# Optimization experiments

Measured on AMD Instinct MI355X. Metric: run time of the kernel, lower is better.

## Reference

```python
import jax, jax.numpy as jnp
from jax import lax
import numpy as np

B = 2048; IMG = 28; K = 3; CIN = 1; HC = 32; LC = 16; WID = 64; HID = 64
LIS = IMG - 3 * (K - 1)           # 22: latent image size
FLAT = LIS * LIS * HC             # 15488
BLK = WID * LC                    # 1024: hypernet block size
T1 = 10.0; T0 = 0.0; NSTEP = 20   # fixed-step RK4 replaces adaptive dopri5
VAR = 0.1                         # p_z0 diagonal covariance


def _conv(x, w, b):  # w: [Cout,Cin,k,k], VALID conv, stride 1
    y = lax.conv_general_dilated(x, w, (1, 1), 'VALID',
                                 dimension_numbers=('NCHW', 'OIHW', 'NCHW'))
    return y + b[None, :, None, None]


def _convT(x, w, b):  # w: [Cin,Cout,k,k] (pytorch ConvTranspose2d layout)
    wf = jnp.flip(w, (2, 3)).transpose(1, 0, 2, 3)  # -> OIHW, spatially flipped
    y = lax.conv_general_dilated(x, wf, (1, 1), [(K - 1, K - 1), (K - 1, K - 1)],
                                 dimension_numbers=('NCHW', 'OIHW', 'NCHW'))
    return y + b[None, :, None, None]


def _forward(x, c0w, c0b, c1w, c1b, c2w, c2b, elw, elb, dlw, dlb,
             t0w, t0b, t1w, t1b, t2w, t2b, h1w, h1b, h2w, h2b, h3w, h3b):
    # ---- encoder (dropout in eval = identity) ----
    h = jnp.tanh(_conv(x, c0w, c0b))
    h = jnp.tanh(_conv(h, c1w, c1b))
    h = jnp.tanh(_conv(h, c2w, c2b))
    z1 = h.reshape(h.shape[0], -1) @ elw + elb          # [B, LC]
    # ---- decoder ----
    d = jnp.tanh(z1 @ dlw + dlb)                         # [B, FLAT]
    d = d.reshape(-1, HC, LIS, LIS)
    d = jnp.tanh(_convT(d, t0w, t0b))
    d = jnp.tanh(_convT(d, t1w, t1b))
    recon = _convT(d, t2w, t2b)                          # [B, CIN, 28, 28]

    # ---- CNF vector field with analytic trace ----
    def hyper(t):
        p = jnp.tanh(jnp.reshape(jnp.asarray(t, jnp.float32), (1, 1)) @ h1w + h1b)
        p = jnp.tanh(p @ h2w + h2b)
        p = (p @ h3w + h3b).reshape(-1)
        W = p[:BLK].reshape(WID, LC)
        U = p[BLK:2 * BLK].reshape(WID, LC) * jax.nn.sigmoid(p[2 * BLK:3 * BLK].reshape(WID, LC))
        Bb = p[3 * BLK:]                                 # [WID]
        return W, Bb, U

    def f(t, z):
        W, Bb, U = hyper(t)
        hh = jnp.tanh(jnp.einsum('bd,wd->wb', z, W) + Bb[:, None])   # [WID, B]
        dz = jnp.einsum('wb,wd->bd', hh, U) / WID                     # [B, LC]
        s = jnp.sum(W * U, axis=1)                                    # [WID]: sum_i W_w[i]U_w[i]
        tr = jnp.mean((1.0 - hh * hh) * s[:, None], axis=0)           # [B] analytic trace
        return dz, -tr[:, None]

    dt = (T0 - T1) / NSTEP

    def step(state, i):
        z, lp = state
        t = T1 + i * dt
        k1z, k1l = f(t, z)
        k2z, k2l = f(t + 0.5 * dt, z + 0.5 * dt * k1z)
        k3z, k3l = f(t + 0.5 * dt, z + 0.5 * dt * k2z)
        k4z, k4l = f(t + dt, z + dt * k3z)
        z = z + dt / 6.0 * (k1z + 2 * k2z + 2 * k3z + k4z)
        lp = lp + dt / 6.0 * (k1l + 2 * k2l + 2 * k3l + k4l)
        return (z, lp), None

    lp1 = jnp.zeros((z1.shape[0], 1), z1.dtype)
    (z0, lp0), _ = lax.scan(step, (z1, lp1), jnp.arange(NSTEP, dtype=jnp.float32))

    # MultivariateNormal(0, 0.1*I) log_prob
    logp = -0.5 * (LC * jnp.log(2 * jnp.pi) + LC * jnp.log(VAR) + jnp.sum(z0 * z0, -1) / VAR)
    x_probs = jnp.mean(logp - lp0[:, 0])
    return recon, x_probs


def setup_inputs() -> dict:
    key = jax.random.key(0)
    ks = jax.random.split(key, 16)
    n = jax.random.normal
    s = jnp.float32(0.05)
    z = jnp.zeros
    OUT3 = 3 * BLK + WID
    return {
        'x': n(ks[0], (B, CIN, IMG, IMG), jnp.float32),
        'c0w': n(ks[1], (HC, CIN, K, K)) * s, 'c0b': z((HC,)),
        'c1w': n(ks[2], (HC, HC, K, K)) * s, 'c1b': z((HC,)),
        'c2w': n(ks[3], (HC, HC, K, K)) * s, 'c2b': z((HC,)),
        'elw': n(ks[4], (FLAT, LC)) * s, 'elb': z((LC,)),
        'dlw': n(ks[5], (LC, FLAT)) * s, 'dlb': z((FLAT,)),
        't0w': n(ks[6], (HC, HC, K, K)) * s, 't0b': z((HC,)),
        't1w': n(ks[7], (HC, HC, K, K)) * s, 't1b': z((HC,)),
        't2w': n(ks[8], (HC, CIN, K, K)) * s, 't2b': z((CIN,)),
        'h1w': n(ks[9], (1, HID)) * s, 'h1b': z((HID,)),
        'h2w': n(ks[10], (HID, HID)) * s, 'h2b': z((HID,)),
        'h3w': n(ks[11], (HID, OUT3)) * s, 'h3b': z((OUT3,)),
    }


def reference(x, c0w, c0b, c1w, c1b, c2w, c2b, elw, elb, dlw, dlb,
              t0w, t0b, t1w, t1b, t2w, t2b, h1w, h1b, h2w, h2b, h3w, h3b):
    return _forward(x, c0w, c0b, c1w, c1b, c2w, c2b, elw, elb, dlw, dlb,
                    t0w, t0b, t1w, t1b, t2w, t2b, h1w, h1b, h2w, h2b, h3w, h3b)
```

## Files before the change

kernel.cpp:

```cpp
#include <hip/hip_runtime.h>
#include <math.h>

#define Bsz 2048

using bf16x8 = __attribute__((ext_vector_type(8))) short;
using f32x4  = __attribute__((ext_vector_type(4))) float;

__device__ __forceinline__ float fast_tanh(float x){
    float e = __expf(2.0f * x);
    return 1.0f - 2.0f / (e + 1.0f);
}
__device__ __forceinline__ float fast_sigmoid(float x){
    return 1.0f / (1.0f + __expf(-x));
}
__device__ __forceinline__ unsigned short f2b(float f){
    union { float f; unsigned u; } v; v.f = f;
    unsigned r = v.u + 0x7FFFu + ((v.u >> 16) & 1u);
    return (unsigned short)(r >> 16);
}
__device__ __forceinline__ float b2f(unsigned short s){
    union { unsigned u; float f; } v; v.u = ((unsigned)s) << 16;
    return v.f;
}

__device__ __forceinline__ float stage_t(int sidx){
    int i  = sidx >> 2, st = sidx & 3;
    float t = 10.0f - 0.5f * (float)i;
    if (st == 1 || st == 2) t -= 0.25f;
    else if (st == 3)       t -= 0.5f;
    return t;
}

__global__ void k_prep(const float* __restrict__ c1w, const float* __restrict__ c2w,
                       const float* __restrict__ t0w, const float* __restrict__ t1w,
                       const float* __restrict__ elw, const float* __restrict__ dlw,
                       const float* __restrict__ elb,
                       unsigned short* __restrict__ wc1, unsigned short* __restrict__ wc2,
                       unsigned short* __restrict__ wt0, unsigned short* __restrict__ wt1,
                       unsigned short* __restrict__ elwT, unsigned short* __restrict__ dlwT,
                       float* __restrict__ z1, int full){
    int gsz = gridDim.x * 256;
    for (int i = blockIdx.x*256 + threadIdx.x; i < 9216; i += gsz){
        int ci = i & 31, co = (i >> 5) & 31, s = i >> 10;
        wc1[i] = f2b(c1w[(co*32 + ci)*9 + s]);
        wc2[i] = f2b(c2w[(co*32 + ci)*9 + s]);
        wt0[i] = f2b(t0w[(ci*32 + co)*9 + (8 - s)]);
        wt1[i] = f2b(t1w[(ci*32 + co)*9 + (8 - s)]);
    }
    if (!full) return;
    for (int i = blockIdx.x*256 + threadIdx.x; i < 32768; i += gsz)
        z1[i] = elb[i & 15];
    for (int i = blockIdx.x*256 + threadIdx.x; i < 247808; i += gsz){
        int l = i / 15488, f2 = i - l*15488;
        int pos = f2 >> 5, ci = f2 & 31;
        elwT[i] = f2b(elw[(ci*484 + pos)*16 + l]);
    }
    for (int i = blockIdx.x*256 + threadIdx.x; i < 247808; i += gsz){
        int f2 = i >> 4, l = i & 15;
        int pos = f2 >> 5, ci = f2 & 31;
        dlwT[i] = f2b(dlw[l*15488 + ci*484 + pos]);
    }
}

__global__ void __launch_bounds__(256)
k_conv0(const float* __restrict__ x, const float* __restrict__ c0w,
        const float* __restrict__ c0b, unsigned short* __restrict__ A0,
        int cb, int CH){
    int gid = blockIdx.x*256 + threadIdx.x;
    if (gid >= CH*676) return;
    int b = gid / 676, pos = gid - b*676;
    int y = pos / 26, xx = pos - y*26;
    const float* xin = x + (size_t)(cb + b)*784;
    float v[9];
#pragma unroll
    for (int r = 0; r < 3; r++)
#pragma unroll
        for (int s = 0; s < 3; s++)
            v[r*3+s] = xin[(y+r)*28 + xx + s];
    unsigned short* ob = A0 + (size_t)b*21632 + pos*32;
#pragma unroll
    for (int g = 0; g < 8; g++){
        float a0 = c0b[g*4+0], a1 = c0b[g*4+1], a2 = c0b[g*4+2], a3 = c0b[g*4+3];
#pragma unroll
        for (int k = 0; k < 9; k++){
            a0 += v[k] * c0w[(g*4+0)*9 + k];
            a1 += v[k] * c0w[(g*4+1)*9 + k];
            a2 += v[k] * c0w[(g*4+2)*9 + k];
            a3 += v[k] * c0w[(g*4+3)*9 + k];
        }
        ushort4 o;
        o.x = f2b(fast_tanh(a0)); o.y = f2b(fast_tanh(a1));
        o.z = f2b(fast_tanh(a2)); o.w = f2b(fast_tanh(a3));
        *(ushort4*)(ob + g*4) = o;
    }
}

template<int IL, int OL, int OW, int OOFF, int INS, int OUTS>
__global__ void __launch_bounds__(256)
k_convM(const unsigned short* __restrict__ in, const unsigned short* __restrict__ wg,
        const float* __restrict__ bias, unsigned short* __restrict__ out, int CH){
    constexpr int N  = OL * OL;
    constexpr int NT = (N + 15) / 16;
    const int tid = threadIdx.x;
    const int wave = tid >> 6, lane = tid & 63;
    const int q = lane >> 4, nn = lane & 15;
    const int nw = gridDim.x * 4;

    bf16x8 af[2][9];
#pragma unroll
    for (int mt = 0; mt < 2; mt++)
#pragma unroll
        for (int s = 0; s < 9; s++)
            af[mt][s] = *(const bf16x8*)(wg + s*1024 + (mt*16 + nn)*32 + q*8);
    float4 bc0 = *(const float4*)(bias + q*4);
    float4 bc1 = *(const float4*)(bias + 16 + q*4);

    for (int t = blockIdx.x*4 + wave; t < CH*NT; t += nw){
        int img = t / NT, tt = t - img*NT;
        const unsigned short* inb = in + (size_t)img * INS;
        unsigned short* outb = out + (size_t)img * OUTS;
        int pos = tt*16 + nn;
        int pc  = pos < N ? pos : N - 1;
        int oy = pc / OL, ox = pc - oy*OL;
        const unsigned short* ib = inb + (oy*IL + ox)*32 + q*8;
        f32x4 acc0 = {0.f,0.f,0.f,0.f}, acc1 = {0.f,0.f,0.f,0.f};
#pragma unroll
        for (int r = 0; r < 3; r++){
            bf16x8 b0 = *(const bf16x8*)(ib + (r*IL + 0)*32);
            bf16x8 b1 = *(const bf16x8*)(ib + (r*IL + 1)*32);
            bf16x8 b2 = *(const bf16x8*)(ib + (r*IL + 2)*32);
            acc0 = __builtin_amdgcn_mfma_f32_16x16x32_bf16(af[0][r*3+0], b0, acc0, 0,0,0);
            acc1 = __builtin_amdgcn_mfma_f32_16x16x32_bf16(af[1][r*3+0], b0, acc1, 0,0,0);
            acc0 = __builtin_amdgcn_mfma_f32_16x16x32_bf16(af[0][r*3+1], b1, acc0, 0,0,0);
            acc1 = __builtin_amdgcn_mfma_f32_16x16x32_bf16(af[1][r*3+1], b1, acc1, 0,0,0);
            acc0 = __builtin_amdgcn_mfma_f32_16x16x32_bf16(af[0][r*3+2], b2, acc0, 0,0,0);
            acc1 = __builtin_amdgcn_mfma_f32_16x16x32_bf16(af[1][r*3+2], b2, acc1, 0,0,0);
        }
        if (pos < N){
            int opix = oy*OW + ox + OOFF;
            ushort4 o0, o1;
            o0.x = f2b(fast_tanh(acc0[0] + bc0.x)); o0.y = f2b(fast_tanh(acc0[1] + bc0.y));
            o0.z = f2b(fast_tanh(acc0[2] + bc0.z)); o0.w = f2b(fast_tanh(acc0[3] + bc0.w));
            o1.x = f2b(fast_tanh(acc1[0] + bc1.x)); o1.y = f2b(fast_tanh(acc1[1] + bc1.y));
            o1.z = f2b(fast_tanh(acc1[2] + bc1.z)); o1.w = f2b(fast_tanh(acc1[3] + bc1.w));
            *(ushort4*)(outb + opix*32 + q*4)      = o0;
            *(ushort4*)(outb + opix*32 + 16 + q*4) = o1;
        }
    }
}

__global__ void __launch_bounds__(256)
k_encg(const unsigned short* __restrict__ A2, const unsigned short* __restrict__ elwT,
       float* __restrict__ z1, int cb, int CH){
    int wave = threadIdx.x >> 6, lane = threadIdx.x & 63;
    int q = lane >> 4, nn = lane & 15;
    int imgb = blockIdx.x*16;
    const unsigned short* ap = A2 + (size_t)(imgb + nn)*15488 + q*8;
    const unsigned short* bp = elwT + (size_t)nn*15488 + q*8;
    f32x4 acc = {0.f,0.f,0.f,0.f};
    int s0 = blockIdx.y*121;
#pragma unroll 2
    for (int s = s0 + wave; s < s0 + 121; s += 4){
        bf16x8 a = *(const bf16x8*)(ap + s*32);
        bf16x8 b = *(const bf16x8*)(bp + s*32);
        acc = __builtin_amdgcn_mfma_f32_16x16x32_bf16(a, b, acc, 0,0,0);
    }
    float* zp = z1 + (size_t)(cb + imgb)*16;
#pragma unroll
    for (int i = 0; i < 4; i++)
        atomicAdd(zp + (q*4 + i)*16 + nn, acc[i]);
}

__global__ void __launch_bounds__(256)
k_halo(unsigned short* __restrict__ D0, unsigned short* __restrict__ D1, int CH){
    int gid = blockIdx.x*256 + threadIdx.x;
    uint4 zq = {0,0,0,0};
    if (gid < CH*676){
        int img = gid / 676, px = gid - img*676;
        int y = px / 26, x = px - y*26;
        if (y < 2 || y >= 24 || x < 2 || x >= 24){
            uint4* p = (uint4*)(D0 + (size_t)img*21632 + px*32);
            p[0] = zq; p[1] = zq; p[2] = zq; p[3] = zq;
        }
    } else {
        int g2 = gid - CH*676;
        if (g2 >= CH*784) return;
        int img = g2 / 784, px = g2 - img*784;
        int y = px / 28, x = px - y*28;
        if (y < 2 || y >= 26 || x < 2 || x >= 26){
            uint4* p = (uint4*)(D1 + (size_t)img*25088 + px*32);
            p[0] = zq; p[1] = zq; p[2] = zq; p[3] = zq;
        }
    }
}

__global__ void __launch_bounds__(256)
k_decg(const float* __restrict__ z1, const unsigned short* __restrict__ dlwT,
       const float* __restrict__ dlb, unsigned short* __restrict__ D0,
       int cb, int CH){
    __shared__ float zl[256];
    int tid = threadIdx.x, ib = blockIdx.y;
    zl[tid] = z1[(size_t)(cb + ib*16 + (tid >> 4))*16 + (tid & 15)];
    __syncthreads();
    int ci = tid & 31, po = tid >> 5;
    int pos = blockIdx.x*8 + po;
    if (pos >= 484) return;
    int y = pos / 22, xx = pos - y*22;
    float bias = dlb[ci*484 + pos];
    const unsigned short* w = dlwT + (size_t)(pos*32 + ci)*16;
    bf16x8 w0 = *(const bf16x8*)(w);
    bf16x8 w1 = *(const bf16x8*)(w + 8);
    float wf[16];
#pragma unroll
    for (int j = 0; j < 8; j++){
        wf[j]   = b2f((unsigned short)w0[j]);
        wf[8+j] = b2f((unsigned short)w1[j]);
    }
    int opix = ((y+2)*26 + xx + 2)*32 + ci;
#pragma unroll 1
    for (int i = 0; i < 16; i++){
        float a = bias;
#pragma unroll
        for (int l = 0; l < 16; l++) a += zl[i*16 + l] * wf[l];
        D0[(size_t)(ib*16 + i)*21632 + opix] = f2b(fast_tanh(a));
    }
}

__global__ void __launch_bounds__(256)
k_convT2(const unsigned short* __restrict__ D2, const float* __restrict__ t2w,
         const float* __restrict__ t2b, float* __restrict__ out, int cb, int CH){
    int gid = blockIdx.x*256 + threadIdx.x;
    if (gid >= CH*784) return;
    int b = gid / 784, o = gid - b*784;
    int y = o / 28, xx = o - y*28;
    const unsigned short* db = D2 + (size_t)b*21632;
    float a = t2b[0];
#pragma unroll
    for (int r = 0; r < 3; r++){
        int iy = y + r - 2;
        if ((unsigned)iy >= 26u) continue;
#pragma unroll
        for (int s = 0; s < 3; s++){
            int ix = xx + s - 2;
            if ((unsigned)ix >= 26u) continue;
            const unsigned short* pp = db + (iy*26 + ix)*32;
            int wi = (2-r)*3 + (2-s);
#pragma unroll
            for (int g = 0; g < 4; g++){
                bf16x8 h = *(const bf16x8*)(pp + g*8);
#pragma unroll
                for (int j = 0; j < 8; j++)
                    a += b2f((unsigned short)h[j]) * t2w[(g*8+j)*9 + wi];
            }
        }
    }
    out[(size_t)(cb + b)*784 + o] = a;
}

template<int LOUT, int INW, int OUTW, int OUTOFF>
__device__ __forceinline__ void conv_gemm(const unsigned short* __restrict__ Wg,
                                          const float* __restrict__ bias,
                                          const unsigned short* inL,
                                          unsigned short* outL, int tid){
    constexpr int N  = LOUT * LOUT;
    constexpr int NT = (N + 15) / 16;
    const int lane  = tid & 63;
    const int wave  = tid >> 6;
    const int mtile = wave & 1;
    const int quad  = lane >> 4;
    const int nn    = lane & 15;
    bf16x8 afr[9];
    const unsigned short* wp = Wg + (mtile*16 + nn)*32 + quad*8;
#pragma unroll
    for (int s = 0; s < 9; s++)
        afr[s] = *(const bf16x8*)(wp + s*1024);
    float4 bco = *(const float4*)(bias + mtile*16 + quad*4);
    for (int t = (wave >> 1); t < NT; t += 2){
        int pos = t*16 + nn;
        int pc  = pos < N ? pos : N - 1;
        int y = pc / LOUT, x = pc - y*LOUT;
        const unsigned short* ib = inL + (y*INW + x)*32 + quad*8;
        f32x4 acc = {0.f, 0.f, 0.f, 0.f};
#pragma unroll
        for (int r = 0; r < 3; r++)
#pragma unroll
            for (int s = 0; s < 3; s++)
                acc = __builtin_amdgcn_mfma_f32_16x16x32_bf16(
                        afr[r*3+s], *(const bf16x8*)(ib + (r*INW + s)*32), acc, 0, 0, 0);
        if (pos < N){
            ushort4 o;
            o.x = f2b(fast_tanh(acc[0] + bco.x));
            o.y = f2b(fast_tanh(acc[1] + bco.y));
            o.z = f2b(fast_tanh(acc[2] + bco.z));
            o.w = f2b(fast_tanh(acc[3] + bco.w));
            int opix = y*OUTW + x + OUTOFF;
            *(ushort4*)(outL + opix*32 + mtile*16 + quad*4) = o;
        }
    }
}

__global__ void __launch_bounds__(256)
k_enc_f(const float* __restrict__ x,
        const float* __restrict__ c0w, const float* __restrict__ c0b,
        const unsigned short* __restrict__ wc1, const float* __restrict__ c1b,
        const unsigned short* __restrict__ wc2, const float* __restrict__ c2b,
        const float* __restrict__ elw, const float* __restrict__ elb,
        float* __restrict__ z1){
    __shared__ float X[784];
    __shared__ __align__(16) unsigned short H0[21632];
    __shared__ __align__(16) unsigned short H1[18432];
    __shared__ __align__(16) unsigned short H2[15488];
    __shared__ float red[16*17];
    const int tid = threadIdx.x, b = blockIdx.x;
    for (int i = tid; i < 784; i += 256) X[i] = x[b*784 + i];
    __syncthreads();
    for (int pos = tid; pos < 676; pos += 256){
        int y = pos / 26, xx = pos - y*26;
        float v[9];
#pragma unroll
        for (int r = 0; r < 3; r++)
#pragma unroll
            for (int s = 0; s < 3; s++)
                v[r*3+s] = X[(y+r)*28 + xx + s];
#pragma unroll
        for (int g = 0; g < 8; g++){
            float a0 = c0b[g*4+0], a1 = c0b[g*4+1], a2 = c0b[g*4+2], a3 = c0b[g*4+3];
#pragma unroll
            for (int k = 0; k < 9; k++){
                a0 += v[k] * c0w[(g*4+0)*9 + k];
                a1 += v[k] * c0w[(g*4+1)*9 + k];
                a2 += v[k] * c0w[(g*4+2)*9 + k];
                a3 += v[k] * c0w[(g*4+3)*9 + k];
            }
            ushort4 o;
            o.x = f2b(fast_tanh(a0)); o.y = f2b(fast_tanh(a1));
            o.z = f2b(fast_tanh(a2)); o.w = f2b(fast_tanh(a3));
            *(ushort4*)(H0 + pos*32 + g*4) = o;
        }
    }
    __syncthreads();
    conv_gemm<24, 26, 24, 0>(wc1, c1b, H0, H1, tid);
    __syncthreads();
    conv_gemm<22, 24, 22, 0>(wc2, c2b, H1, H2, tid);
    __syncthreads();
    {
        int fg = tid >> 4, l = tid & 15;
        float a = 0.f;
        for (int ci = 0; ci < 32; ci++)
            for (int pos = fg; pos < 484; pos += 16)
                a += b2f(H2[pos*32 + ci]) * elw[(ci*484 + pos)*16 + l];
        red[fg*17 + l] = a;
        __syncthreads();
        if (tid < 16){
            float s = elb[tid];
#pragma unroll
            for (int g = 0; g < 16; g++) s += red[g*17 + tid];
            z1[b*16 + tid] = s;
        }
    }
}

__global__ void __launch_bounds__(256)
k_dec_f(const float* __restrict__ z1,
        const float* __restrict__ dlw, const float* __restrict__ dlb,
        const unsigned short* __restrict__ wt0, const float* __restrict__ t0b,
        const unsigned short* __restrict__ wt1, const float* __restrict__ t1b,
        const float* __restrict__ t2w, const float* __restrict__ t2b,
        float* __restrict__ out){
    __shared__ __align__(16) unsigned short D0[21632];
    __shared__ __align__(16) unsigned short D1[25088];
    __shared__ __align__(16) unsigned short D2[28800];
    const int tid = threadIdx.x, b = blockIdx.x;
    {
        uint4 zq = {0,0,0,0};
        for (int i = tid; i < 2704; i += 256) ((uint4*)D0)[i] = zq;
        for (int i = tid; i < 3136; i += 256) ((uint4*)D1)[i] = zq;
        for (int i = tid; i < 3600; i += 256) ((uint4*)D2)[i] = zq;
    }
    float zz[16];
#pragma unroll
    for (int l = 0; l < 16; l++) zz[l] = z1[b*16 + l];
    __syncthreads();
    for (int f = tid; f < 15488; f += 256){
        float a = dlb[f];
#pragma unroll
        for (int l = 0; l < 16; l++) a += zz[l] * dlw[l*15488 + f];
        int ci = f / 484, pos = f - ci*484;
        int y = pos / 22, xx = pos - y*22;
        D0[((y+2)*26 + xx + 2)*32 + ci] = f2b(fast_tanh(a));
    }
    __syncthreads();
    conv_gemm<24, 26, 28, 58>(wt0, t0b, D0, D1, tid);
    __syncthreads();
    conv_gemm<26, 28, 30, 62>(wt1, t1b, D1, D2, tid);
    __syncthreads();
    for (int o = tid; o < 784; o += 256){
        int y = o / 28, xx = o - y*28;
        float a = t2b[0];
#pragma unroll
        for (int r = 0; r < 3; r++)
#pragma unroll
            for (int s = 0; s < 3; s++){
                const unsigned short* pp = D2 + ((y+r)*30 + xx + s)*32;
                int wi = (2-r)*3 + (2-s);
#pragma unroll
                for (int g = 0; g < 4; g++){
                    bf16x8 h = *(const bf16x8*)(pp + g*8);
#pragma unroll
                    for (int j = 0; j < 8; j++)
                        a += b2f((unsigned short)h[j]) * t2w[(g*8+j)*9 + wi];
                }
            }
        out[(size_t)b*784 + o] = a;
    }
}

__global__ void __launch_bounds__(64)
k_hyp1(const float* __restrict__ h1w, const float* __restrict__ h1b,
       const float* __restrict__ h2w, const float* __restrict__ h2b,
       float* __restrict__ p2ws){
    __shared__ float p1l[64];
    int sidx = blockIdx.x, tid = threadIdx.x;
    float t = stage_t(sidx);
    p1l[tid] = fast_tanh(t * h1w[tid] + h1b[tid]);
    __syncthreads();
    float a0 = h2b[tid], a1 = 0.f, a2 = 0.f, a3 = 0.f;
#pragma unroll
    for (int k = 0; k < 64; k += 4){
        a0 += p1l[k]   * h2w[(k)*64   + tid];
        a1 += p1l[k+1] * h2w[(k+1)*64 + tid];
        a2 += p1l[k+2] * h2w[(k+2)*64 + tid];
        a3 += p1l[k+3] * h2w[(k+3)*64 + tid];
    }
    p2ws[sidx*64 + tid] = fast_tanh((a0 + a1) + (a2 + a3));
}

__global__ void __launch_bounds__(256)
k_hyp2(const float* __restrict__ p2ws, const float* __restrict__ h3w,
       const float* __restrict__ h3b, float* __restrict__ p3ws){
    __shared__ float p2l[64];
    int sidx = blockIdx.y, tid = threadIdx.x;
    if (tid < 64) p2l[tid] = p2ws[sidx*64 + tid];
    __syncthreads();
    int m = blockIdx.x*256 + tid;
    if (m >= 3136) return;
    const float* hp = h3w + m;
    float a0 = h3b[m], a1 = 0.f, a2 = 0.f, a3 = 0.f;
#pragma unroll
    for (int k = 0; k < 64; k += 4){
        a0 += p2l[k]   * hp[(size_t)(k)*3136];
        a1 += p2l[k+1] * hp[(size_t)(k+1)*3136];
        a2 += p2l[k+2] * hp[(size_t)(k+2)*3136];
        a3 += p2l[k+3] * hp[(size_t)(k+3)*3136];
    }
    p3ws[(size_t)sidx*3200 + m] = (a0 + a1) + (a2 + a3);
}

__global__ void __launch_bounds__(256)
k_hyp3(const float* __restrict__ p3ws, float* __restrict__ hyp){
    __shared__ float partial[256];
    int sidx = blockIdx.x, tid = threadIdx.x;
    const float* p3 = p3ws + (size_t)sidx*3200;
    float* g = hyp + (size_t)sidx*2304;
    int m0 = tid*4;
    float4 w4 = *(const float4*)(p3 + m0);
    float4 a4 = *(const float4*)(p3 + 1024 + m0);
    float4 s4 = *(const float4*)(p3 + 2048 + m0);
    float4 u4;
    u4.x = a4.x * fast_sigmoid(s4.x);
    u4.y = a4.y * fast_sigmoid(s4.y);
    u4.z = a4.z * fast_sigmoid(s4.z);
    u4.w = a4.w * fast_sigmoid(s4.w);
    *(float4*)(g + m0) = w4;
    g[1024 + ((m0+0) & 15)*64 + ((m0+0) >> 4)] = u4.x;
    g[1024 + ((m0+1) & 15)*64 + ((m0+1) >> 4)] = u4.y;
    g[1024 + ((m0+2) & 15)*64 + ((m0+2) >> 4)] = u4.z;
    g[1024 + ((m0+3) & 15)*64 + ((m0+3) >> 4)] = u4.w;
    partial[tid] = w4.x*u4.x + w4.y*u4.y + w4.z*u4.z + w4.w*u4.w;
    __syncthreads();
    if (tid < 64){
        g[2048 + tid] = p3[3072 + tid];
        g[2112 + tid] = partial[tid*4] + partial[tid*4+1]
                      + partial[tid*4+2] + partial[tid*4+3];
    }
}

__global__ void k_hyper(const float* __restrict__ h1w, const float* __restrict__ h1b,
                        const float* __restrict__ h2w, const float* __restrict__ h2b,
                        const float* __restrict__ h3w, const float* __restrict__ h3b,
                        float* __restrict__ hyp){
    int sidx = blockIdx.x;
    float t = stage_t(sidx);
    __shared__ float p1[64], p2[64];
    __shared__ float p3[3136];
    int tid = threadIdx.x;
    if (tid < 64) p1[tid] = fast_tanh(t * h1w[tid] + h1b[tid]);
    __syncthreads();
    if (tid < 64){
        float a = h2b[tid];
#pragma unroll
        for (int k = 0; k < 64; k++) a += p1[k] * h2w[k*64 + tid];
        p2[tid] = fast_tanh(a);
    }
    __syncthreads();
    for (int m = tid; m < 3136; m += 256){
        float a = h3b[m];
#pragma unroll
        for (int k = 0; k < 64; k++) a += p2[k] * h3w[k*3136 + m];
        p3[m] = a;
    }
    __syncthreads();
    float* g = hyp + (size_t)sidx * 2304;
    for (int m = tid; m < 1024; m += 256){
        g[m] = p3[m];
        float u = p3[1024 + m] * fast_sigmoid(p3[2048 + m]);
        g[1024 + (m & 15)*64 + (m >> 4)] = u;
        p3[1024 + m] = u;
    }
    if (tid < 64) g[2048 + tid] = p3[3072 + tid];
    __syncthreads();
    if (tid < 64){
        float s = 0.f;
#pragma unroll
        for (int d = 0; d < 16; d++) s += p3[tid*16 + d] * p3[1024 + tid*16 + d];
        g[2112 + tid] = s;
    }
}

struct PF { float4 Wr[4]; float4 Ur[4]; float Bb, sw; };

__device__ __forceinline__ void load_pf(const float* __restrict__ g,
                                        int lane, int q, int d, PF& p){
    const float4* w4 = (const float4*)(g + lane*16);
    p.Wr[0] = w4[0]; p.Wr[1] = w4[1]; p.Wr[2] = w4[2]; p.Wr[3] = w4[3];
    const float4* u4 = (const float4*)(g + 1024 + d*64 + q*16);
    p.Ur[0] = u4[0]; p.Ur[1] = u4[1]; p.Ur[2] = u4[2]; p.Ur[3] = u4[3];
    p.Bb = g[2048 + lane];
    p.sw = g[2112 + lane];
}

__global__ void __launch_bounds__(64)
k_cnf(const float* __restrict__ z1, const float* __restrict__ hyp,
      float* __restrict__ part){
    __shared__ __align__(16) float zsl[16];
    __shared__ __align__(16) float hhl[64];
    const int lane = threadIdx.x;
    const int q = lane >> 4, d = lane & 15;
    const float dt = -0.5f;

    float z  = z1[(size_t)blockIdx.x*16 + d];
    float zs = z;
    float lp = 0.f, zacc = 0.f, lacc = 0.f;
    if (lane < 16) zsl[lane] = zs;

    PF cur, nxt;
    load_pf(hyp, lane, q, d, cur);

    for (int sidx = 0; sidx < 80; sidx++){
        __syncthreads();
        if (sidx < 79) load_pf(hyp + (size_t)(sidx + 1)*2304, lane, q, d, nxt);

        const float4* zp = (const float4*)zsl;
        float4 z0 = zp[0], z1v = zp[1], z2 = zp[2], z3 = zp[3];
        float a = cur.Bb;
        a += z0.x*cur.Wr[0].x + z0.y*cur.Wr[0].y + z0.z*cur.Wr[0].z + z0.w*cur.Wr[0].w;
        a += z1v.x*cur.Wr[1].x + z1v.y*cur.Wr[1].y + z1v.z*cur.Wr[1].z + z1v.w*cur.Wr[1].w;
        a += z2.x*cur.Wr[2].x + z2.y*cur.Wr[2].y + z2.z*cur.Wr[2].z + z2.w*cur.Wr[2].w;
        a += z3.x*cur.Wr[3].x + z3.y*cur.Wr[3].y + z3.z*cur.Wr[3].z + z3.w*cur.Wr[3].w;
        float hh = fast_tanh(a);
        float e = (1.f - hh*hh) * cur.sw;
#pragma unroll
        for (int off = 1; off < 64; off <<= 1)
            e += __shfl_xor(e, off);
        hhl[lane] = hh;
        __syncthreads();

        const float4* hp = (const float4*)(hhl + q*16);
        float4 h0 = hp[0], h1 = hp[1], h2 = hp[2], h3 = hp[3];
        float dzp = 0.f;
        dzp += h0.x*cur.Ur[0].x + h0.y*cur.Ur[0].y + h0.z*cur.Ur[0].z + h0.w*cur.Ur[0].w;
        dzp += h1.x*cur.Ur[1].x + h1.y*cur.Ur[1].y + h1.z*cur.Ur[1].z + h1.w*cur.Ur[1].w;
        dzp += h2.x*cur.Ur[2].x + h2.y*cur.Ur[2].y + h2.z*cur.Ur[2].z + h2.w*cur.Ur[2].w;
        dzp += h3.x*cur.Ur[3].x + h3.y*cur.Ur[3].y + h3.z*cur.Ur[3].z + h3.w*cur.Ur[3].w;
        dzp += __shfl_xor(dzp, 16);
        dzp += __shfl_xor(dzp, 32);
        float dz = dzp * (1.f/64.f);
        float dl = -e  * (1.f/64.f);

        int st = sidx & 3;
        float wgt = (st == 0 || st == 3) ? 1.f : 2.f;
        zacc += wgt * dz;
        lacc += wgt * dl;
        if (st < 3){
            float aa = (st == 2) ? 1.0f : 0.5f;
            zs = z + aa * dt * dz;
        } else {
            z  += (dt/6.f) * zacc;
            lp += (dt/6.f) * lacc;
            zs = z;
            zacc = 0.f; lacc = 0.f;
        }
        if (lane < 16) zsl[lane] = zs;
        cur = nxt;
    }

    float sq = z * z;
#pragma unroll
    for (int off = 1; off < 16; off <<= 1) sq += __shfl_xor(sq, off, 16);
    float logp = -0.5f * (16.f*1.8378770664093453f + 16.f*(-2.302585092994046f) + sq*10.f);
    if (lane == 0) part[blockIdx.x] = logp - lp;
}

__global__ void k_final(const float* __restrict__ part, float* __restrict__ out){
    __shared__ float red[256];
    int tid = threadIdx.x;
    float s = 0.f;
#pragma unroll
    for (int k = 0; k < 8; k++) s += part[tid + k*256];
    red[tid] = s;
    __syncthreads();
    for (int st = 128; st > 0; st >>= 1){
        if (tid < st) red[tid] += red[tid + st];
        __syncthreads();
    }
    if (tid == 0) out[1605632] = red[0] * (1.f/2048.f);
}

extern "C" void kernel_launch(void* const* d_in, const int* in_sizes, int n_in,
                              void* d_out, int out_size, void* d_ws, size_t ws_size,
                              hipStream_t stream){
    const float* x   = (const float*)d_in[0];
    const float* c0w = (const float*)d_in[1];
    const float* c0b = (const float*)d_in[2];
    const float* c1w = (const float*)d_in[3];
    const float* c1b = (const float*)d_in[4];
    const float* c2w = (const float*)d_in[5];
    const float* c2b = (const float*)d_in[6];
    const float* elw = (const float*)d_in[7];
    const float* elb = (const float*)d_in[8];
    const float* dlw = (const float*)d_in[9];
    const float* dlb = (const float*)d_in[10];
    const float* t0w = (const float*)d_in[11];
    const float* t0b = (const float*)d_in[12];
    const float* t1w = (const float*)d_in[13];
    const float* t1b = (const float*)d_in[14];
    const float* t2w = (const float*)d_in[15];
    const float* t2b = (const float*)d_in[16];
    const float* h1w = (const float*)d_in[17];
    const float* h1b = (const float*)d_in[18];
    const float* h2w = (const float*)d_in[19];
    const float* h2b = (const float*)d_in[20];
    const float* h3w = (const float*)d_in[21];
    const float* h3b = (const float*)d_in[22];

    float* ws   = (float*)d_ws;
    float* z1   = ws;
    float* hyp  = z1 + 32768;
    float* part = hyp + 184320;
    float* p2ws = part + 2048;
    float* p3ws = p2ws + 5120;
    unsigned short* wc1  = (unsigned short*)(p3ws + 256000);
    unsigned short* wc2  = wc1 + 9216;
    unsigned short* wt0  = wc2 + 9216;
    unsigned short* wt1  = wt0 + 9216;
    unsigned short* elwT = wt1 + 9216;
    unsigned short* dlwT = elwT + 247808;
    unsigned short* act  = dlwT + 247808;
    float* rec  = (float*)d_out;

    const size_t MISC = 2985984;
    int CH = 0;
    const int cands[6] = {2048, 1024, 512, 256, 128, 64};
    for (int c = 0; c < 6; c++){
        size_t need = MISC + (size_t)cands[c] * 111104;
        if (need <= ws_size){ CH = cands[c]; break; }
    }

    if (CH == 0){
        k_hyper<<<80, 256, 0, stream>>>(h1w, h1b, h2w, h2b, h3w, h3b, hyp);
        k_prep <<<64,   256, 0, stream>>>(c1w, c2w, t0w, t1w, elw, dlw, elb,
                                          wc1, wc2, wt0, wt1, wt1, wt1, z1, 0);
        k_enc_f<<<2048, 256, 0, stream>>>(x, c0w, c0b, wc1, c1b, wc2, c2b, elw, elb, z1);
        k_cnf  <<<2048,  64, 0, stream>>>(z1, hyp, part);
        k_dec_f<<<2048, 256, 0, stream>>>(z1, dlw, dlb, wt0, t0b, wt1, t1b, t2w, t2b, rec);
        k_final<<<1,    256, 0, stream>>>(part, rec);
        return;
    }

    k_hyp1<<<80,           64, 0, stream>>>(h1w, h1b, h2w, h2b, p2ws);
    k_hyp2<<<dim3(13,80), 256, 0, stream>>>(p2ws, h3w, h3b, p3ws);
    k_hyp3<<<80,          256, 0, stream>>>(p3ws, hyp);

    k_prep<<<64, 256, 0, stream>>>(c1w, c2w, t0w, t1w, elw, dlw, elb,
                                   wc1, wc2, wt0, wt1, elwT, dlwT, z1, 1);

    unsigned short* R0 = act;
    unsigned short* R1 = R0 + (size_t)CH*21632;
    unsigned short* R2 = R1 + (size_t)CH*18432;
    unsigned short* D1 = R1;

    for (int cb = 0; cb < Bsz; cb += CH){
        k_conv0<<<(CH*676 + 255)/256, 256, 0, stream>>>(x, c0w, c0b, R0, cb, CH);
        k_convM<26,24,24, 0, 21632, 18432><<<(CH*36 + 15)/16, 256, 0, stream>>>(R0, wc1, c1b, R1, CH);
        k_convM<24,22,22, 0, 18432, 15488><<<(CH*31 + 15)/16, 256, 0, stream>>>(R1, wc2, c2b, R2, CH);
        k_encg<<<dim3(CH/16, 4), 256, 0, stream>>>(R2, elwT, z1, cb, CH);
        k_halo<<<(CH*1460 + 255)/256, 256, 0, stream>>>(R0, D1, CH);
        k_decg<<<dim3(61, CH/16), 256, 0, stream>>>(z1, dlwT, dlb, R0, cb, CH);
        k_convM<26,24,28,58, 21632, 25088><<<(CH*36 + 15)/16, 256, 0, stream>>>(R0, wt0, t0b, D1, CH);
        k_convM<28,26,26, 0, 25088, 21632><<<(CH*43 + 15)/16, 256, 0, stream>>>(D1, wt1, t1b, R0, CH);
        k_convT2<<<(CH*784 + 255)/256, 256, 0, stream>>>(R0, t2w, t2b, rec, cb, CH);
    }
    k_cnf  <<<2048,  64, 0, stream>>>(z1, hyp, part);
    k_final<<<1,    256, 0, stream>>>(part, rec);
}
```

Measured before the change: 662.6 us.

## Batch CNF integration across 16 samples per block using bf16 MFMA

Replaces the per-sample CNF RK4 kernel, which used one 64-thread block per sample with scalar dot products, by a kernel that handles 16 samples per block. Both matmuls (z·Wᵀ and hh·U) run as bf16 16x16x32 MFMA instructions. k_hyp3 now packs the hypernetwork W and U into bf16 MFMA fragment layouts and precomputes the summed trace term, so the trace becomes stot minus the sum of tanh² terms. The path cuts the grid from 2048 to 128 blocks and drops barriers, but it loses precision through bf16 rounding of z, W, U and tanh. The in-loop shared-memory handoffs between lanes now have no __syncthreads; within a single wavefront this may be safe but is fragile. The fallback path still calls the fp32 kernel, which reads the old 2304-stride hyp layout, while k_hyp3 now writes a 2048-stride layout that only the main path may populate.

```diff
diff --git a/kernel.cpp b/kernel.cpp
--- a/kernel.cpp
+++ b/kernel.cpp
@@ -458,30 +458,57 @@
 
 __global__ void __launch_bounds__(256)
 k_hyp3(const float* __restrict__ p3ws, float* __restrict__ hyp){
-    __shared__ float partial[256];
+    __shared__ float sred[64];
     int sidx = blockIdx.x, tid = threadIdx.x;
     const float* p3 = p3ws + (size_t)sidx*3200;
-    float* g = hyp + (size_t)sidx*2304;
-    int m0 = tid*4;
-    float4 w4 = *(const float4*)(p3 + m0);
-    float4 a4 = *(const float4*)(p3 + 1024 + m0);
-    float4 s4 = *(const float4*)(p3 + 2048 + m0);
-    float4 u4;
-    u4.x = a4.x * fast_sigmoid(s4.x);
-    u4.y = a4.y * fast_sigmoid(s4.y);
-    u4.z = a4.z * fast_sigmoid(s4.z);
-    u4.w = a4.w * fast_sigmoid(s4.w);
-    *(float4*)(g + m0) = w4;
-    g[1024 + ((m0+0) & 15)*64 + ((m0+0) >> 4)] = u4.x;
-    g[1024 + ((m0+1) & 15)*64 + ((m0+1) >> 4)] = u4.y;
-    g[1024 + ((m0+2) & 15)*64 + ((m0+2) >> 4)] = u4.z;
-    g[1024 + ((m0+3) & 15)*64 + ((m0+3) >> 4)] = u4.w;
-    partial[tid] = w4.x*u4.x + w4.y*u4.y + w4.z*u4.z + w4.w*u4.w;
-    __syncthreads();
-    if (tid < 64){
-        g[2048 + tid] = p3[3072 + tid];
-        g[2112 + tid] = partial[tid*4] + partial[tid*4+1]
-                      + partial[tid*4+2] + partial[tid*4+3];
+    float* g = hyp + (size_t)sidx*2048;
+    unsigned short* gW = (unsigned short*)g;
+    unsigned short* gU = (unsigned short*)(g + 1024);
+
+    {
+        int lane = tid & 63, c = tid >> 6;
+        int q = lane >> 4, m = lane & 15;
+        ushort4 o0 = {0,0,0,0}, o1 = {0,0,0,0};
+        if (q < 2){
+            const float* wp = p3 + (c*16 + m)*16 + q*8;
+            o0.x = f2b(wp[0]); o0.y = f2b(wp[1]); o0.z = f2b(wp[2]); o0.w = f2b(wp[3]);
+            o1.x = f2b(wp[4]); o1.y = f2b(wp[5]); o1.z = f2b(wp[6]); o1.w = f2b(wp[7]);
+        }
+        *(ushort4*)(gW + tid*8)     = o0;
+        *(ushort4*)(gW + tid*8 + 4) = o1;
+    }
+    if (tid < 128){
+        int lane = tid & 63, kb = tid >> 6;
+        int q = lane >> 4, d = lane & 15;
+        unsigned short uo[8];
+#pragma unroll
+        for (int j = 0; j < 8; j++){
+            int w = kb*32 + q*8 + j;
+            float u = p3[1024 + w*16 + d] * fast_sigmoid(p3[2048 + w*16 + d]);
+            uo[j] = f2b(u);
+        }
+        *(ushort4*)(gU + tid*8)     = *(ushort4*)&uo[0];
+        *(ushort4*)(gU + tid*8 + 4) = *(ushort4*)&uo[4];
+    } else if (tid < 192){
+        int w = tid - 128;
+        g[1536 + w] = p3[3072 + w];
+    } else {
+        int w = tid - 192;
+        float s = 0.f;
+#pragma unroll
+        for (int d = 0; d < 16; d++){
+            float u = p3[1024 + w*16 + d] * fast_sigmoid(p3[2048 + w*16 + d]);
+            s += p3[w*16 + d] * u;
+        }
+        g[1600 + w] = s;
+        sred[w] = s;
+    }
+    __syncthreads();
+    if (tid == 0){
+        float st = 0.f;
+#pragma unroll
+        for (int w = 0; w < 64; w++) st += sred[w];
+        g[1664] = st;
     }
 }
 
@@ -527,8 +554,134 @@
     }
 }
 
+struct PM {
+    bf16x8 Wf[4];
+    bf16x8 Uf[2];
+    float4 Bbf[4];
+    float4 sf[4];
+    float stot;
+};
+__device__ __forceinline__ void loadPM(const float* __restrict__ g, int lane, int q, PM& p){
+    const unsigned short* gW = (const unsigned short*)g;
+    const unsigned short* gU = (const unsigned short*)(g + 1024);
+#pragma unroll
+    for (int c = 0; c < 4; c++)
+        p.Wf[c] = *(const bf16x8*)(gW + (c*64 + lane)*8);
+#pragma unroll
+    for (int kb = 0; kb < 2; kb++)
+        p.Uf[kb] = *(const bf16x8*)(gU + (kb*64 + lane)*8);
+#pragma unroll
+    for (int c = 0; c < 4; c++){
+        p.Bbf[c] = *(const float4*)(g + 1536 + c*16 + q*4);
+        p.sf[c]  = *(const float4*)(g + 1600 + c*16 + q*4);
+    }
+    p.stot = g[1664];
+}
+
+__global__ void __launch_bounds__(64)
+k_cnfM(const float* __restrict__ z1, const float* __restrict__ hyp,
+       float* __restrict__ part){
+    __shared__ __align__(16) float zsf[384];
+    __shared__ __align__(16) unsigned short hhT[16*72];
+    __shared__ float trl[16];
+    const int lane = threadIdx.x;
+    const int q = lane >> 4, d = lane & 15;
+    const float dt = -0.5f;
+
+    float z[4], zacc[4], lacc[4], lp[4];
+#pragma unroll
+    for (int i = 0; i < 4; i++){
+        z[i] = z1[(size_t)(blockIdx.x*16 + q*4 + i)*16 + d];
+        zacc[i] = 0.f; lacc[i] = 0.f; lp[i] = 0.f;
+        zsf[(q*4 + i)*20 + d] = z[i];
+    }
+    PM cur, nxt;
+    loadPM(hyp, lane, q, cur);
+
+    for (int sidx = 0; sidx < 80; sidx++){
+        bf16x8 zb;
+        if (q < 2){
+            float4 za = *(const float4*)(zsf + d*20 + q*8);
+            float4 zc = *(const float4*)(zsf + d*20 + q*8 + 4);
+            zb[0]=(short)f2b(za.x); zb[1]=(short)f2b(za.y);
+            zb[2]=(short)f2b(za.z); zb[3]=(short)f2b(za.w);
+            zb[4]=(short)f2b(zc.x); zb[5]=(short)f2b(zc.y);
+            zb[6]=(short)f2b(zc.z); zb[7]=(short)f2b(zc.w);
+        } else {
+            bf16x8 zz2 = {0,0,0,0,0,0,0,0}; zb = zz2;
+        }
+        f32x4 h0 = {0,0,0,0}, h1 = {0,0,0,0}, h2 = {0,0,0,0}, h3 = {0,0,0,0};
+        h0 = __builtin_amdgcn_mfma_f32_16x16x32_bf16(cur.Wf[0], zb, h0, 0,0,0);
+        h1 = __builtin_amdgcn_mfma_f32_16x16x32_bf16(cur.Wf[1], zb, h1, 0,0,0);
+        h2 = __builtin_amdgcn_mfma_f32_16x16x32_bf16(cur.Wf[2], zb, h2, 0,0,0);
+        h3 = __builtin_amdgcn_mfma_f32_16x16x32_bf16(cur.Wf[3], zb, h3, 0,0,0);
+        if (sidx < 79) loadPM(hyp + (size_t)(sidx + 1)*2048, lane, q, nxt);
+
+        float partial = 0.f;
+        f32x4 hc[4] = {h0, h1, h2, h3};
+#pragma unroll
+        for (int c = 0; c < 4; c++){
+            ushort4 o;
+            float t0 = fast_tanh(hc[c][0] + cur.Bbf[c].x);
+            float t1 = fast_tanh(hc[c][1] + cur.Bbf[c].y);
+            float t2 = fast_tanh(hc[c][2] + cur.Bbf[c].z);
+            float t3 = fast_tanh(hc[c][3] + cur.Bbf[c].w);
+            partial += t0*t0*cur.sf[c].x + t1*t1*cur.sf[c].y
+                     + t2*t2*cur.sf[c].z + t3*t3*cur.sf[c].w;
+            o.x = f2b(t0); o.y = f2b(t1); o.z = f2b(t2); o.w = f2b(t3);
+            *(ushort4*)(hhT + d*72 + c*16 + q*4) = o;
+        }
+        partial += __shfl_xor(partial, 16);
+        partial += __shfl_xor(partial, 32);
+        if (lane < 16) trl[lane] = (cur.stot - partial) * (1.f/64.f);
+
+        bf16x8 a20 = *(const bf16x8*)(hhT + d*72 + q*8);
+        bf16x8 a21 = *(const bf16x8*)(hhT + d*72 + 32 + q*8);
+        f32x4 dzac = {0,0,0,0};
+        dzac = __builtin_amdgcn_mfma_f32_16x16x32_bf16(a20, cur.Uf[0], dzac, 0,0,0);
+        dzac = __builtin_amdgcn_mfma_f32_16x16x32_bf16(a21, cur.Uf[1], dzac, 0,0,0);
+
+        int st = sidx & 3;
+        float wgt = (st == 0 || st == 3) ? 1.f : 2.f;
+#pragma unroll
+        for (int i = 0; i < 4; i++){
+            float dz = dzac[i] * (1.f/64.f);
+            float dl = -trl[q*4 + i];
+            zacc[i] += wgt * dz;
+            lacc[i] += wgt * dl;
+            float zsv;
+            if (st < 3){
+                float aa = (st == 2) ? 1.0f : 0.5f;
+                zsv = z[i] + aa * dt * dz;
+            } else {
+                z[i]  += (dt/6.f) * zacc[i];
+                lp[i] += (dt/6.f) * lacc[i];
+                zsv = z[i];
+                zacc[i] = 0.f; lacc[i] = 0.f;
+            }
+            zsf[(q*4 + i)*20 + d] = zsv;
+        }
+        cur = nxt;
+    }
+    float sq[4];
+#pragma unroll
+    for (int i = 0; i < 4; i++) sq[i] = z[i]*z[i];
+#pragma unroll
+    for (int off = 1; off < 16; off <<= 1){
+#pragma unroll
+        for (int i = 0; i < 4; i++) sq[i] += __shfl_xor(sq[i], off, 16);
+    }
+    if (d == 0){
+#pragma unroll
+        for (int i = 0; i < 4; i++){
+            float logp = -0.5f * (16.f*1.8378770664093453f
+                                 + 16.f*(-2.302585092994046f) + sq[i]*10.f);
+            part[blockIdx.x*16 + q*4 + i] = logp - lp[i];
+        }
+    }
+}
+
 struct PF { float4 Wr[4]; float4 Ur[4]; float Bb, sw; };
-
 __device__ __forceinline__ void load_pf(const float* __restrict__ g,
                                         int lane, int q, int d, PF& p){
     const float4* w4 = (const float4*)(g + lane*16);
@@ -538,28 +691,23 @@
     p.Bb = g[2048 + lane];
     p.sw = g[2112 + lane];
 }
-
 __global__ void __launch_bounds__(64)
-k_cnf(const float* __restrict__ z1, const float* __restrict__ hyp,
-      float* __restrict__ part){
+k_cnf_f(const float* __restrict__ z1, const float* __restrict__ hyp,
+        float* __restrict__ part){
     __shared__ __align__(16) float zsl[16];
     __shared__ __align__(16) float hhl[64];
     const int lane = threadIdx.x;
     const int q = lane >> 4, d = lane & 15;
     const float dt = -0.5f;
-
     float z  = z1[(size_t)blockIdx.x*16 + d];
     float zs = z;
     float lp = 0.f, zacc = 0.f, lacc = 0.f;
     if (lane < 16) zsl[lane] = zs;
-
     PF cur, nxt;
     load_pf(hyp, lane, q, d, cur);
-
     for (int sidx = 0; sidx < 80; sidx++){
         __syncthreads();
         if (sidx < 79) load_pf(hyp + (size_t)(sidx + 1)*2304, lane, q, d, nxt);
-
         const float4* zp = (const float4*)zsl;
         float4 z0 = zp[0], z1v = zp[1], z2 = zp[2], z3 = zp[3];
         float a = cur.Bb;
@@ -574,7 +722,6 @@
             e += __shfl_xor(e, off);
         hhl[lane] = hh;
         __syncthreads();
-
         const float4* hp = (const float4*)(hhl + q*16);
         float4 h0 = hp[0], h1 = hp[1], h2 = hp[2], h3 = hp[3];
         float dzp = 0.f;
@@ -586,7 +733,6 @@
         dzp += __shfl_xor(dzp, 32);
         float dz = dzp * (1.f/64.f);
         float dl = -e  * (1.f/64.f);
-
         int st = sidx & 3;
         float wgt = (st == 0 || st == 3) ? 1.f : 2.f;
         zacc += wgt * dz;
@@ -603,7 +749,6 @@
         if (lane < 16) zsl[lane] = zs;
         cur = nxt;
     }
-
     float sq = z * z;
 #pragma unroll
     for (int off = 1; off < 16; off <<= 1) sq += __shfl_xor(sq, off, 16);
@@ -681,7 +826,7 @@
         k_prep <<<64,   256, 0, stream>>>(c1w, c2w, t0w, t1w, elw, dlw, elb,
                                           wc1, wc2, wt0, wt1, wt1, wt1, z1, 0);
         k_enc_f<<<2048, 256, 0, stream>>>(x, c0w, c0b, wc1, c1b, wc2, c2b, elw, elb, z1);
-        k_cnf  <<<2048,  64, 0, stream>>>(z1, hyp, part);
+        k_cnf_f<<<2048,  64, 0, stream>>>(z1, hyp, part);
         k_dec_f<<<2048, 256, 0, stream>>>(z1, dlw, dlb, wt0, t0b, wt1, t1b, t2w, t2b, rec);
         k_final<<<1,    256, 0, stream>>>(part, rec);
         return;
@@ -710,6 +855,6 @@
         k_convM<28,26,26, 0, 25088, 21632><<<(CH*43 + 15)/16, 256, 0, stream>>>(D1, wt1, t1b, R0, CH);
         k_convT2<<<(CH*784 + 255)/256, 256, 0, stream>>>(R0, t2w, t2b, rec, cb, CH);
     }
-    k_cnf  <<<2048,  64, 0, stream>>>(z1, hyp, part);
-    k_final<<<1,    256, 0, stream>>>(part, rec);
-}
+    k_cnfM <<<128,  64, 0, stream>>>(z1, hyp, part);
+    k_final<<<1,   256, 0, stream>>>(part, rec);
+}
```

Result: no change. 652.2 us (-1.6%).
